# Kernel tuning notes

Hardware: AMD Instinct MI355X
Metric: run time of the kernel (lower is better)

## Reference

```python
import jax, jax.numpy as jnp
import numpy as np

N = 50000
E = 800000
F_IN = 128
HID = 128
NCLS = 64


def setup_inputs() -> dict:
    key = jax.random.key(0)
    ks = jax.random.split(key, 10)
    x = jax.random.normal(ks[0], (N, F_IN), dtype=jnp.float32)
    edge_index = jax.random.randint(ks[1], (2, E), 0, N, dtype=jnp.int64)
    def w(k, fi, fo):
        return jax.random.normal(k, (fi, fo), dtype=jnp.float32) / np.sqrt(fi)
    return {
        "x": x,
        "edge_index": edge_index,
        "W1": w(ks[2], F_IN, HID), "b1": jnp.zeros((HID,), jnp.float32),
        "W2": w(ks[3], HID, HID), "b2": jnp.zeros((HID,), jnp.float32),
        "W3": w(ks[4], HID, HID), "b3": jnp.zeros((HID,), jnp.float32),
        "W4": w(ks[5], HID, NCLS), "b4": jnp.zeros((NCLS,), jnp.float32),
    }


def _build_graph(edge_index, n):
    # PyG GCNConv default: add self loops, symmetric normalization D^-1/2 (A+I) D^-1/2
    loops = jnp.arange(n, dtype=edge_index.dtype)
    row = jnp.concatenate([edge_index[0], loops])  # source
    col = jnp.concatenate([edge_index[1], loops])  # destination
    deg = jax.ops.segment_sum(jnp.ones_like(col, dtype=jnp.float32), col, num_segments=n)
    dinv = jnp.where(deg > 0, jax.lax.rsqrt(deg), 0.0)
    norm = dinv[row] * dinv[col]  # [E+N]
    return row, col, norm


def _gcn_layer(x, row, col, norm, W, b, n):
    h = x @ W                                    # [N, out]
    msg = h[row] * norm[:, None]                 # gather + scale, [E+N, out]
    out = jax.ops.segment_sum(msg, col, num_segments=n)  # scatter-add
    return out + b


def reference(x, edge_index, W1, b1, W2, b2, W3, b3, W4, b4):
    n = x.shape[0]
    row, col, norm = _build_graph(edge_index, n)
    h = jax.nn.relu(_gcn_layer(x, row, col, norm, W1, b1, n))
    h = jax.nn.relu(_gcn_layer(h, row, col, norm, W2, b2, n))
    h = jax.nn.relu(_gcn_layer(h, row, col, norm, W3, b3, n))
    return _gcn_layer(h, row, col, norm, W4, b4, n)
```

## Files before the change

kernel.cpp:

```cpp
#include <hip/hip_runtime.h>
#include <hip/hip_fp16.h>
#include <type_traits>

#define N_NODES 50000
#define N_EDGES 800000
#define WIN_BITS 9
#define WIN 512
#define NBUK ((N_NODES + WIN - 1) / WIN)
#define BCAP 16384

typedef _Float16 half8 __attribute__((ext_vector_type(8)));
typedef float floatx4 __attribute__((ext_vector_type(4)));

__device__ inline void acc8(float* a, half8 v) {
    const __half2* p = (const __half2*)&v;
    float2 f0 = __half22float2(p[0]);
    float2 f1 = __half22float2(p[1]);
    float2 f2 = __half22float2(p[2]);
    float2 f3 = __half22float2(p[3]);
    a[0] += f0.x; a[1] += f0.y; a[2] += f1.x; a[3] += f1.y;
    a[4] += f2.x; a[5] += f2.y; a[6] += f3.x; a[7] += f3.y;
}

__global__ __launch_bounds__(256) void p0_wfrag(
        const int* __restrict__ ei, int* __restrict__ gcur,
        unsigned* __restrict__ arena, int E,
        const float* __restrict__ W1, const float* __restrict__ W2,
        const float* __restrict__ W3, const float* __restrict__ W4,
        _Float16* __restrict__ Wf1, _Float16* __restrict__ Wf2,
        _Float16* __restrict__ Wf3, _Float16* __restrict__ Wf4) {
    int tid = threadIdx.x;
    if (blockIdx.x >= 512) {
        int b = blockIdx.x - 512;
        const float* W; _Float16* Wf; int FO; int lb;
        if (b < 8)       { W = W1; Wf = Wf1; FO = 128; lb = b; }
        else if (b < 16) { W = W2; Wf = Wf2; FO = 128; lb = b - 8; }
        else if (b < 24) { W = W3; Wf = Wf3; FO = 128; lb = b - 16; }
        else             { W = W4; Wf = Wf4; FO = 64;  lb = b - 24; }
        int g = lb * 256 + tid;
        if (g >= 16 * FO) return;
        int col = g % FO;
        int sq = g / FO;
        int k0 = sq * 8;
        half8 hv;
        #pragma unroll
        for (int j = 0; j < 8; ++j)
            hv[j] = (_Float16)W[(size_t)(k0 + j) * FO + col];
        *(half8*)&Wf[(size_t)g * 8] = hv;
        return;
    }
    __shared__ int lcnt[NBUK];
    __shared__ int lbase[NBUK];
    int chunk = (E + 511) / 512;
    int e0 = blockIdx.x * chunk;
    int e1 = e0 + chunk; if (e1 > E) e1 = E;
    for (int b = tid; b < NBUK; b += 256) lcnt[b] = 0;
    __syncthreads();
    for (int e = e0 + tid; e < e1; e += 256) {
        int dst = ei[E + e];
        atomicAdd(&lcnt[dst >> WIN_BITS], 1);
    }
    __syncthreads();
    for (int b = tid; b < NBUK; b += 256) {
        lbase[b] = atomicAdd(&gcur[b], lcnt[b]);
        lcnt[b] = 0;
    }
    __syncthreads();
    for (int e = e0 + tid; e < e1; e += 256) {
        int dst = ei[E + e];
        int src = ei[e];
        int b = dst >> WIN_BITS;
        int pos = lbase[b] + atomicAdd(&lcnt[b], 1);
        if (pos < BCAP)
            arena[(size_t)b * BCAP + pos] = ((unsigned)src << WIN_BITS) | (unsigned)(dst & (WIN - 1));
    }
}

__global__ __launch_bounds__(256) void build_graph(
        const unsigned* __restrict__ arena, const int* __restrict__ gcur,
        int* __restrict__ offsets, float* __restrict__ dinv,
        int* __restrict__ csr_src, int n, int total) {
    __shared__ int cnt[WIN];
    __shared__ int sbuf[256];
    __shared__ int bukoff_s;
    int b = blockIdx.x, tid = threadIdx.x;

    sbuf[tid] = (tid < b) ? gcur[tid] : 0;
    cnt[tid] = 0; cnt[tid + 256] = 0;
    __syncthreads();
    #pragma unroll
    for (int off = 128; off > 0; off >>= 1) {
        if (tid < off) sbuf[tid] += sbuf[tid + off];
        __syncthreads();
    }
    if (tid == 0) bukoff_s = sbuf[0];

    int m = gcur[b]; if (m > BCAP) m = BCAP;
    const unsigned* a = arena + (size_t)b * BCAP;
    for (int i = tid; i < m; i += 256) atomicAdd(&cnt[a[i] & (WIN - 1)], 1);
    __syncthreads();

    int j0 = tid * 2;
    int a0 = cnt[j0], a1 = cnt[j0 + 1];
    int ts = a0 + a1;
    sbuf[tid] = ts;
    __syncthreads();
    for (int off = 1; off < 256; off <<= 1) {
        int u = (tid >= off) ? sbuf[tid - off] : 0;
        __syncthreads();
        sbuf[tid] += u;
        __syncthreads();
    }
    int pre = sbuf[tid] - ts;
    int base = b << WIN_BITS;
    int o0 = bukoff_s + pre, o1 = o0 + a0;
    int d0 = base + j0;
    if (d0 + 1 < n) {
        *(int2*)&offsets[d0] = make_int2(o0, o1);
        *(float2*)&dinv[d0] = make_float2(rsqrtf((float)(a0 + 1)), rsqrtf((float)(a1 + 1)));
    } else if (d0 < n) {
        offsets[d0] = o0;
        dinv[d0] = rsqrtf((float)(a0 + 1));
    }
    __syncthreads();
    cnt[j0] = o0; cnt[j0 + 1] = o1;
    __syncthreads();
    for (int i = tid; i < m; i += 256) {
        unsigned e = a[i];
        int pos = atomicAdd(&cnt[e & (WIN - 1)], 1);
        csr_src[pos] = (int)(e >> WIN_BITS);
    }
    if (b == 0 && tid == 0) offsets[n] = total;
}

__global__ __launch_bounds__(256) void gemm_mfma_kernel(
        const float* __restrict__ x, const _Float16* __restrict__ Wfrag,
        const float* __restrict__ dinv, __half* __restrict__ h, int n) {
    constexpr int FO = 128;
    constexpr int NT = FO / 16;
    int tid = threadIdx.x;
    int ln = tid & 15;
    int q  = (tid >> 4) & 3;
    int w  = tid >> 6;
    int node = blockIdx.x * 64 + w * 16 + ln;
    int nodec = node < n ? node : n - 1;
    const float* xrow = x + (size_t)nodec * 128;

    floatx4 acc[NT];
    #pragma unroll
    for (int t = 0; t < NT; ++t) acc[t] = (floatx4){0.f, 0.f, 0.f, 0.f};

    #pragma unroll
    for (int s = 0; s < 4; ++s) {
        const float* xp = xrow + s * 32 + q * 8;
        float4 a0 = *(const float4*)xp;
        float4 a1 = *(const float4*)(xp + 4);
        half8 xf;
        xf[0] = (_Float16)a0.x; xf[1] = (_Float16)a0.y;
        xf[2] = (_Float16)a0.z; xf[3] = (_Float16)a0.w;
        xf[4] = (_Float16)a1.x; xf[5] = (_Float16)a1.y;
        xf[6] = (_Float16)a1.z; xf[7] = (_Float16)a1.w;
        int sq = s * 4 + q;
        #pragma unroll
        for (int t = 0; t < NT; ++t) {
            half8 wf = *(const half8*)&Wfrag[(size_t)(sq * FO + t * 16 + ln) * 8];
            acc[t] = __builtin_amdgcn_mfma_f32_16x16x32_f16(wf, xf, acc[t], 0, 0, 0);
        }
    }

    if (node < n) {
        float dv = dinv[node];
        __half* hrow = h + (size_t)node * FO;
        #pragma unroll
        for (int t = 0; t < NT; ++t) {
            __half2 p[2];
            p[0] = __float22half2_rn(make_float2(acc[t][0] * dv, acc[t][1] * dv));
            p[1] = __float22half2_rn(make_float2(acc[t][2] * dv, acc[t][3] * dv));
            *(uint2*)&hrow[t * 16 + q * 4] = *(const uint2*)p;
        }
    }
}

template<int FO>
__global__ __launch_bounds__(512) void fused_agg_gemm(
        const _Float16* __restrict__ hin, const int* __restrict__ offsets,
        const int* __restrict__ csr_src, const float* __restrict__ dinv,
        const float* __restrict__ bias, const _Float16* __restrict__ Wfrag,
        __half* __restrict__ hout, int n) {
    constexpr int NT  = FO / 16;
    constexpr int TPW = NT / 2;
    __shared__ _Float16 aggL[64 * 136];

    int tid = threadIdx.x;
    int w = tid >> 6;
    int lane = tid & 63;
    int qw = lane >> 4, sl = lane & 15;
    float4 bb0 = *(const float4*)&bias[sl * 8];
    float4 bb1 = *(const float4*)&bias[sl * 8 + 4];

    for (int pp = 0; pp < 4; ++pp) {
        int c0 = blockIdx.x * 64 + w * 8 + pp * 2;
        if (c0 >= n) break;
        int c1 = c0 + 1;
        bool v1 = c1 < n;
        c0 = __builtin_amdgcn_readfirstlane(c0);
        c1 = __builtin_amdgcn_readfirstlane(c1);

        float a0[8] = {0.f, 0.f, 0.f, 0.f, 0.f, 0.f, 0.f, 0.f};
        float a1[8] = {0.f, 0.f, 0.f, 0.f, 0.f, 0.f, 0.f, 0.f};
        if (qw == 0) acc8(a0, *(const half8*)&hin[(size_t)c0 * 128 + sl * 8]);
        if (v1 && qw == 0) acc8(a1, *(const half8*)&hin[(size_t)c1 * 128 + sl * 8]);

        int i0 = offsets[c0], e0 = offsets[c0 + 1];
        int i1 = v1 ? offsets[c1] : 0, e1 = v1 ? offsets[c1 + 1] : 0;

        while (i0 + 3 < e0 && i1 + 3 < e1) {
            int sa = csr_src[i0 + qw];
            int sb = csr_src[i1 + qw];
            half8 va = *(const half8*)&hin[(size_t)sa * 128 + sl * 8];
            half8 vb = *(const half8*)&hin[(size_t)sb * 128 + sl * 8];
            acc8(a0, va);
            acc8(a1, vb);
            i0 += 4; i1 += 4;
        }
        for (; i0 + 3 < e0; i0 += 4) {
            int sa = csr_src[i0 + qw];
            acc8(a0, *(const half8*)&hin[(size_t)sa * 128 + sl * 8]);
        }
        if (i0 + qw < e0) {
            int sa = csr_src[i0 + qw];
            acc8(a0, *(const half8*)&hin[(size_t)sa * 128 + sl * 8]);
        }
        for (; i1 + 3 < e1; i1 += 4) {
            int sb = csr_src[i1 + qw];
            acc8(a1, *(const half8*)&hin[(size_t)sb * 128 + sl * 8]);
        }
        if (v1 && i1 + qw < e1) {
            int sb = csr_src[i1 + qw];
            acc8(a1, *(const half8*)&hin[(size_t)sb * 128 + sl * 8]);
        }

        #pragma unroll
        for (int k = 0; k < 8; ++k) {
            a0[k] += __shfl_xor(a0[k], 16);
            a0[k] += __shfl_xor(a0[k], 32);
            a1[k] += __shfl_xor(a1[k], 16);
            a1[k] += __shfl_xor(a1[k], 32);
        }
        if (qw == 0) {
            {
                float dc = dinv[c0];
                half8 hv;
                hv[0] = (_Float16)fmaxf(fmaf(a0[0], dc, bb0.x), 0.f);
                hv[1] = (_Float16)fmaxf(fmaf(a0[1], dc, bb0.y), 0.f);
                hv[2] = (_Float16)fmaxf(fmaf(a0[2], dc, bb0.z), 0.f);
                hv[3] = (_Float16)fmaxf(fmaf(a0[3], dc, bb0.w), 0.f);
                hv[4] = (_Float16)fmaxf(fmaf(a0[4], dc, bb1.x), 0.f);
                hv[5] = (_Float16)fmaxf(fmaf(a0[5], dc, bb1.y), 0.f);
                hv[6] = (_Float16)fmaxf(fmaf(a0[6], dc, bb1.z), 0.f);
                hv[7] = (_Float16)fmaxf(fmaf(a0[7], dc, bb1.w), 0.f);
                *(half8*)&aggL[(size_t)(w * 8 + pp * 2) * 136 + sl * 8] = hv;
            }
            if (v1) {
                float dc = dinv[c1];
                half8 hv;
                hv[0] = (_Float16)fmaxf(fmaf(a1[0], dc, bb0.x), 0.f);
                hv[1] = (_Float16)fmaxf(fmaf(a1[1], dc, bb0.y), 0.f);
                hv[2] = (_Float16)fmaxf(fmaf(a1[2], dc, bb0.z), 0.f);
                hv[3] = (_Float16)fmaxf(fmaf(a1[3], dc, bb0.w), 0.f);
                hv[4] = (_Float16)fmaxf(fmaf(a1[4], dc, bb1.x), 0.f);
                hv[5] = (_Float16)fmaxf(fmaf(a1[5], dc, bb1.y), 0.f);
                hv[6] = (_Float16)fmaxf(fmaf(a1[6], dc, bb1.z), 0.f);
                hv[7] = (_Float16)fmaxf(fmaf(a1[7], dc, bb1.w), 0.f);
                *(half8*)&aggL[(size_t)(w * 8 + pp * 2 + 1) * 136 + sl * 8] = hv;
            }
        }
    }
    __syncthreads();

    int ng = w & 3, cg = w >> 2;
    int ln = tid & 15;
    int q  = (tid >> 4) & 3;
    int nl = ng * 16 + ln;
    int node = blockIdx.x * 64 + nl;

    floatx4 acc[TPW];
    #pragma unroll
    for (int t = 0; t < TPW; ++t) acc[t] = (floatx4){0.f, 0.f, 0.f, 0.f};

    #pragma unroll
    for (int s = 0; s < 4; ++s) {
        half8 xf = *(const half8*)&aggL[(size_t)nl * 136 + s * 32 + q * 8];
        int sq = s * 4 + q;
        #pragma unroll
        for (int t = 0; t < TPW; ++t) {
            int T = cg * TPW + t;
            half8 wf = *(const half8*)&Wfrag[(size_t)(sq * FO + T * 16 + ln) * 8];
            acc[t] = __builtin_amdgcn_mfma_f32_16x16x32_f16(wf, xf, acc[t], 0, 0, 0);
        }
    }

    if (node < n) {
        float dv = dinv[node];
        __half* hrow = hout + (size_t)node * FO;
        #pragma unroll
        for (int t = 0; t < TPW; ++t) {
            int T = cg * TPW + t;
            __half2 p[2];
            p[0] = __float22half2_rn(make_float2(acc[t][0] * dv, acc[t][1] * dv));
            p[1] = __float22half2_rn(make_float2(acc[t][2] * dv, acc[t][3] * dv));
            *(uint2*)&hrow[T * 16 + q * 4] = *(const uint2*)p;
        }
    }
}

__global__ __launch_bounds__(256) void agg64_kernel(
        const _Float16* __restrict__ h, const int* __restrict__ offsets,
        const int* __restrict__ csr_src, const float* __restrict__ dinv,
        const float* __restrict__ bias, float* __restrict__ out, int n) {
    int lane = threadIdx.x & 63;
    int o = lane >> 3, sl = lane & 7;
    int c = (blockIdx.x << 2) + (threadIdx.x >> 6);
    if (c >= n) return;
    c = __builtin_amdgcn_readfirstlane(c);
    float acc[8] = {0.f, 0.f, 0.f, 0.f, 0.f, 0.f, 0.f, 0.f};
    if (o == 0)
        acc8(acc, *(const half8*)&h[(size_t)c * 64 + sl * 8]);
    int s = offsets[c], e = offsets[c + 1];
    int i = s;
    for (; i + 15 < e; i += 16) {
        int sa = csr_src[i + o];
        int sb = csr_src[i + 8 + o];
        half8 va = *(const half8*)&h[(size_t)sa * 64 + sl * 8];
        half8 vb = *(const half8*)&h[(size_t)sb * 64 + sl * 8];
        acc8(acc, va);
        acc8(acc, vb);
    }
    for (; i + 7 < e; i += 8) {
        int sa = csr_src[i + o];
        acc8(acc, *(const half8*)&h[(size_t)sa * 64 + sl * 8]);
    }
    if (i + o < e) {
        int sa = csr_src[i + o];
        acc8(acc, *(const half8*)&h[(size_t)sa * 64 + sl * 8]);
    }
    #pragma unroll
    for (int k = 0; k < 8; ++k) {
        acc[k] += __shfl_xor(acc[k], 8);
        acc[k] += __shfl_xor(acc[k], 16);
        acc[k] += __shfl_xor(acc[k], 32);
    }
    if (o == 0) {
        float dc = dinv[c];
        float4 bb0 = *(const float4*)&bias[sl * 8];
        float4 bb1 = *(const float4*)&bias[sl * 8 + 4];
        float4 o0, o1;
        o0.x = fmaf(acc[0], dc, bb0.x); o0.y = fmaf(acc[1], dc, bb0.y);
        o0.z = fmaf(acc[2], dc, bb0.z); o0.w = fmaf(acc[3], dc, bb0.w);
        o1.x = fmaf(acc[4], dc, bb1.x); o1.y = fmaf(acc[5], dc, bb1.y);
        o1.z = fmaf(acc[6], dc, bb1.z); o1.w = fmaf(acc[7], dc, bb1.w);
        float* orow = out + (size_t)c * 64 + sl * 8;
        *(float4*)orow = o0;
        *(float4*)(orow + 4) = o1;
    }
}


extern "C" void kernel_launch(void* const* d_in, const int* in_sizes, int n_in,
                              void* d_out, int out_size, void* d_ws, size_t ws_size,
                              hipStream_t stream) {
    const float* x  = (const float*)d_in[0];
    const int*   ei = (const int*)  d_in[1];
    const float* W1 = (const float*)d_in[2];
    const float* b1 = (const float*)d_in[3];
    const float* W2 = (const float*)d_in[4];
    const float* b2 = (const float*)d_in[5];
    const float* W3 = (const float*)d_in[6];
    const float* b3 = (const float*)d_in[7];
    const float* W4 = (const float*)d_in[8];
    const float* b4 = (const float*)d_in[9];

    const int N = N_NODES, E = N_EDGES;

    char* p = (char*)d_ws;
    auto carve = [&](size_t bytes) {
        char* q = p;
        p += (bytes + 255) & ~(size_t)255;
        return (void*)q;
    };
    int*       offsets = (int*)      carve((size_t)(N + 1) * 4);
    int*       csr_src = (int*)      carve((size_t)E * 4);
    float*     dinv    = (float*)    carve((size_t)N * 4);
    int*       gcur    = (int*)      carve((size_t)NBUK * 4);
    unsigned*  arena   = (unsigned*) carve((size_t)NBUK * BCAP * 4);
    _Float16*  Wf1     = (_Float16*) carve((size_t)16 * 128 * 8 * 2);
    _Float16*  Wf2     = (_Float16*) carve((size_t)16 * 128 * 8 * 2);
    _Float16*  Wf3     = (_Float16*) carve((size_t)16 * 128 * 8 * 2);
    _Float16*  Wf4     = (_Float16*) carve((size_t)16 * 64 * 8 * 2);
    __half*    A1      = (__half*)   carve((size_t)N * 128 * 2);
    __half*    A2      = (__half*)   carve((size_t)N * 128 * 2);

    hipMemsetAsync(gcur, 0, (size_t)NBUK * 4, stream);
    p0_wfrag<<<540, 256, 0, stream>>>(ei, gcur, arena, E,
                                      W1, W2, W3, W4, Wf1, Wf2, Wf3, Wf4);
    build_graph<<<NBUK, 256, 0, stream>>>(arena, gcur, offsets, dinv, csr_src, N, E);

    const int nb64 = (N + 63) / 64;

    gemm_mfma_kernel<<<nb64, 256, 0, stream>>>(x, Wf1, dinv, A1, N);
    fused_agg_gemm<128><<<nb64, 512, 0, stream>>>((const _Float16*)A1, offsets, csr_src, dinv, b1, Wf2, A2, N);
    fused_agg_gemm<128><<<nb64, 512, 0, stream>>>((const _Float16*)A2, offsets, csr_src, dinv, b2, Wf3, A1, N);
    fused_agg_gemm<64><<<nb64, 512, 0, stream>>>((const _Float16*)A1, offsets, csr_src, dinv, b3, Wf4, A2, N);
    agg64_kernel<<<(N + 3) / 4, 256, 0, stream>>>((const _Float16*)A2, offsets, csr_src, dinv, b4, (float*)d_out, N);
}
```

Measured before the change: 274.1 us.

## Split feature halves across waves and process 8 edges per wave iteration

```diff
diff --git a/kernel.cpp b/kernel.cpp
--- a/kernel.cpp
+++ b/kernel.cpp
@@ -188,18 +188,23 @@
         const float* __restrict__ bias, const _Float16* __restrict__ Wfrag,
         __half* __restrict__ hout, int n) {
     constexpr int NT  = FO / 16;
-    constexpr int TPW = NT / 2;
-    __shared__ _Float16 aggL[64 * 136];
+    constexpr int TPW = NT / 4;
+    __shared__ _Float16 aggL[32 * 136];
 
     int tid = threadIdx.x;
     int w = tid >> 6;
     int lane = tid & 63;
-    int qw = lane >> 4, sl = lane & 15;
-    float4 bb0 = *(const float4*)&bias[sl * 8];
-    float4 bb1 = *(const float4*)&bias[sl * 8 + 4];
+    int g = w & 3;
+    int h = w >> 2;
+    int eo = lane >> 3;
+    int sf = lane & 7;
+    int foff = h * 64 + sf * 8;
+    float4 bb0 = *(const float4*)&bias[foff];
+    float4 bb1 = *(const float4*)&bias[foff + 4];
+    const _Float16* hf = hin + foff;
 
     for (int pp = 0; pp < 4; ++pp) {
-        int c0 = blockIdx.x * 64 + w * 8 + pp * 2;
+        int c0 = blockIdx.x * 32 + g * 8 + pp * 2;
         if (c0 >= n) break;
         int c1 = c0 + 1;
         bool v1 = c1 < n;
@@ -208,46 +213,49 @@
 
         float a0[8] = {0.f, 0.f, 0.f, 0.f, 0.f, 0.f, 0.f, 0.f};
         float a1[8] = {0.f, 0.f, 0.f, 0.f, 0.f, 0.f, 0.f, 0.f};
-        if (qw == 0) acc8(a0, *(const half8*)&hin[(size_t)c0 * 128 + sl * 8]);
-        if (v1 && qw == 0) acc8(a1, *(const half8*)&hin[(size_t)c1 * 128 + sl * 8]);
+        if (eo == 0) acc8(a0, *(const half8*)&hf[(size_t)c0 * 128]);
+        if (v1 && eo == 0) acc8(a1, *(const half8*)&hf[(size_t)c1 * 128]);
 
         int i0 = offsets[c0], e0 = offsets[c0 + 1];
         int i1 = v1 ? offsets[c1] : 0, e1 = v1 ? offsets[c1 + 1] : 0;
 
-        while (i0 + 3 < e0 && i1 + 3 < e1) {
-            int sa = csr_src[i0 + qw];
-            int sb = csr_src[i1 + qw];
-            half8 va = *(const half8*)&hin[(size_t)sa * 128 + sl * 8];
-            half8 vb = *(const half8*)&hin[(size_t)sb * 128 + sl * 8];
+        while (i0 + 7 < e0 && i1 + 7 < e1) {
+            int sa = csr_src[i0 + eo];
+            int sb = csr_src[i1 + eo];
+            half8 va = *(const half8*)&hf[(size_t)sa * 128];
+            half8 vb = *(const half8*)&hf[(size_t)sb * 128];
             acc8(a0, va);
             acc8(a1, vb);
-            i0 += 4; i1 += 4;
-        }
-        for (; i0 + 3 < e0; i0 += 4) {
-            int sa = csr_src[i0 + qw];
-            acc8(a0, *(const half8*)&hin[(size_t)sa * 128 + sl * 8]);
-        }
-        if (i0 + qw < e0) {
-            int sa = csr_src[i0 + qw];
-            acc8(a0, *(const half8*)&hin[(size_t)sa * 128 + sl * 8]);
-        }
-        for (; i1 + 3 < e1; i1 += 4) {
-            int sb = csr_src[i1 + qw];
-            acc8(a1, *(const half8*)&hin[(size_t)sb * 128 + sl * 8]);
-        }
-        if (v1 && i1 + qw < e1) {
-            int sb = csr_src[i1 + qw];
-            acc8(a1, *(const half8*)&hin[(size_t)sb * 128 + sl * 8]);
+            i0 += 8; i1 += 8;
+        }
+        for (; i0 + 7 < e0; i0 += 8) {
+            int sa = csr_src[i0 + eo];
+            acc8(a0, *(const half8*)&hf[(size_t)sa * 128]);
+        }
+        if (i0 + eo < e0) {
+            int sa = csr_src[i0 + eo];
+            acc8(a0, *(const half8*)&hf[(size_t)sa * 128]);
+        }
+        for (; i1 + 7 < e1; i1 += 8) {
+            int sb = csr_src[i1 + eo];
+            acc8(a1, *(const half8*)&hf[(size_t)sb * 128]);
+        }
+        if (v1 && i1 + eo < e1) {
+            int sb = csr_src[i1 + eo];
+            acc8(a1, *(const half8*)&hf[(size_t)sb * 128]);
         }
 
         #pragma unroll
         for (int k = 0; k < 8; ++k) {
+            a0[k] += __shfl_xor(a0[k], 8);
             a0[k] += __shfl_xor(a0[k], 16);
             a0[k] += __shfl_xor(a0[k], 32);
+            a1[k] += __shfl_xor(a1[k], 8);
             a1[k] += __shfl_xor(a1[k], 16);
             a1[k] += __shfl_xor(a1[k], 32);
         }
-        if (qw == 0) {
+        if (eo == 0) {
+            int row = g * 8 + pp * 2;
             {
                 float dc = dinv[c0];
                 half8 hv;
@@ -259,7 +267,7 @@
                 hv[5] = (_Float16)fmaxf(fmaf(a0[5], dc, bb1.y), 0.f);
                 hv[6] = (_Float16)fmaxf(fmaf(a0[6], dc, bb1.z), 0.f);
                 hv[7] = (_Float16)fmaxf(fmaf(a0[7], dc, bb1.w), 0.f);
-                *(half8*)&aggL[(size_t)(w * 8 + pp * 2) * 136 + sl * 8] = hv;
+                *(half8*)&aggL[(size_t)row * 136 + foff] = hv;
             }
             if (v1) {
                 float dc = dinv[c1];
@@ -272,17 +280,17 @@
                 hv[5] = (_Float16)fmaxf(fmaf(a1[5], dc, bb1.y), 0.f);
                 hv[6] = (_Float16)fmaxf(fmaf(a1[6], dc, bb1.z), 0.f);
                 hv[7] = (_Float16)fmaxf(fmaf(a1[7], dc, bb1.w), 0.f);
-                *(half8*)&aggL[(size_t)(w * 8 + pp * 2 + 1) * 136 + sl * 8] = hv;
+                *(half8*)&aggL[(size_t)(row + 1) * 136 + foff] = hv;
             }
         }
     }
     __syncthreads();
 
-    int ng = w & 3, cg = w >> 2;
+    int ng = w & 1, cg = w >> 1;
     int ln = tid & 15;
     int q  = (tid >> 4) & 3;
     int nl = ng * 16 + ln;
-    int node = blockIdx.x * 64 + nl;
+    int node = blockIdx.x * 32 + nl;
 
     floatx4 acc[TPW];
     #pragma unroll
@@ -406,10 +414,11 @@
     build_graph<<<NBUK, 256, 0, stream>>>(arena, gcur, offsets, dinv, csr_src, N, E);
 
     const int nb64 = (N + 63) / 64;
+    const int nb32 = (N + 31) / 32;
 
     gemm_mfma_kernel<<<nb64, 256, 0, stream>>>(x, Wf1, dinv, A1, N);
-    fused_agg_gemm<128><<<nb64, 512, 0, stream>>>((const _Float16*)A1, offsets, csr_src, dinv, b1, Wf2, A2, N);
-    fused_agg_gemm<128><<<nb64, 512, 0, stream>>>((const _Float16*)A2, offsets, csr_src, dinv, b2, Wf3, A1, N);
-    fused_agg_gemm<64><<<nb64, 512, 0, stream>>>((const _Float16*)A1, offsets, csr_src, dinv, b3, Wf4, A2, N);
+    fused_agg_gemm<128><<<nb32, 512, 0, stream>>>((const _Float16*)A1, offsets, csr_src, dinv, b1, Wf2, A2, N);
+    fused_agg_gemm<128><<<nb32, 512, 0, stream>>>((const _Float16*)A2, offsets, csr_src, dinv, b2, Wf3, A1, N);
+    fused_agg_gemm<64><<<nb32, 512, 0, stream>>>((const _Float16*)A1, offsets, csr_src, dinv, b3, Wf4, A2, N);
     agg64_kernel<<<(N + 3) / 4, 256, 0, stream>>>((const _Float16*)A2, offsets, csr_src, dinv, b4, (float*)d_out, N);
 }
```

New measurement: 308.7 us. 1.13x slower.
